# Performance work log

Hardware: AMD Instinct MI355X
Metric: run time of the kernel (lower is better)

Reference implementation:

```python
import jax, jax.numpy as jnp
import numpy as np

B, W, N, F_IN = 2, 8, 10000, 5
E = 80000
H = 128


def setup_inputs() -> dict:
    key = jax.random.key(0)
    ks = jax.random.split(key, 16)
    s = 0.05
    inp = {
        "x": jax.random.normal(ks[0], (B, W, N, F_IN), dtype=jnp.float32),
        "edge_index": jax.random.randint(ks[1], (2, E), 0, N, dtype=jnp.int64),
        # GCN layer 1 (in_features -> hidden) and layer 2 (hidden -> hidden)
        "gcn1_w": jax.random.normal(ks[2], (F_IN, H), dtype=jnp.float32) * s,
        "gcn1_b": jnp.zeros((H,), dtype=jnp.float32),
        "gcn2_w": jax.random.normal(ks[3], (H, H), dtype=jnp.float32) * s,
        "gcn2_b": jnp.zeros((H,), dtype=jnp.float32),
        # LSTM (torch gate order: i, f, g, o)
        "lstm_w_ih": jax.random.normal(ks[4], (4 * H, H), dtype=jnp.float32) * s,
        "lstm_w_hh": jax.random.normal(ks[5], (4 * H, H), dtype=jnp.float32) * s,
        "lstm_b_ih": jnp.zeros((4 * H,), dtype=jnp.float32),
        "lstm_b_hh": jnp.zeros((4 * H,), dtype=jnp.float32),
        # Decoder MLP: H -> H//2 -> 1
        "dec_w1": jax.random.normal(ks[6], (H, H // 2), dtype=jnp.float32) * s,
        "dec_b1": jnp.zeros((H // 2,), dtype=jnp.float32),
        "dec_w2": jax.random.normal(ks[7], (H // 2, 1), dtype=jnp.float32) * s,
        "dec_b2": jnp.zeros((1,), dtype=jnp.float32),
    }
    return inp


def _forward(x, edge_index, gcn1_w, gcn1_b, gcn2_w, gcn2_b,
             lstm_w_ih, lstm_w_hh, lstm_b_ih, lstm_b_hh,
             dec_w1, dec_b1, dec_w2, dec_b2):
    b, w, n, f_in = x.shape
    h_dim = gcn1_w.shape[1]
    # --- GCN normalization (PyG GCNConv default: add self-loops, sym-norm) ---
    loop = jnp.arange(n, dtype=edge_index.dtype)
    src = jnp.concatenate([edge_index[0], loop])
    dst = jnp.concatenate([edge_index[1], loop])
    deg = jnp.zeros((n,), x.dtype).at[dst].add(jnp.float32(1.0))
    dinv = jax.lax.rsqrt(deg)
    norm = dinv[src] * dinv[dst]  # (E+N,)

    def gcn(h, wm, bias):
        # h: (BW, N, Fin) -> (BW, N, H). Transform-then-aggregate (linear op).
        ht = h @ wm                                   # (BW, N, H)
        msg = ht[:, src, :] * norm[None, :, None]      # (BW, E+N, H)
        agg = jnp.zeros_like(ht).at[:, dst, :].add(msg)
        return agg + bias

    xf = x.reshape(b * w, n, f_in)
    h = jax.nn.relu(gcn(xf, gcn1_w, gcn1_b))   # dropout is identity at eval
    h = jax.nn.relu(gcn(h, gcn2_w, gcn2_b))

    # (BW, N, H) -> (B, N, W, H) -> (B*N, W, H): per-node temporal sequences
    h = h.reshape(b, w, n, h_dim).transpose(0, 2, 1, 3).reshape(b * n, w, h_dim)

    # --- single-layer LSTM, keep only last hidden state ---
    def step(carry, xt):
        hp, cp = carry
        gates = xt @ lstm_w_ih.T + hp @ lstm_w_hh.T + lstm_b_ih + lstm_b_hh
        i, f, g, o = jnp.split(gates, 4, axis=-1)
        c = jax.nn.sigmoid(f) * cp + jax.nn.sigmoid(i) * jnp.tanh(g)
        hn = jax.nn.sigmoid(o) * jnp.tanh(c)
        return (hn, c), None

    init = (jnp.zeros((b * n, h_dim), x.dtype), jnp.zeros((b * n, h_dim), x.dtype))
    (h_last, _), _ = jax.lax.scan(step, init, h.transpose(1, 0, 2))  # scan over W

    # --- MLP decoder ---
    d = jax.nn.relu(h_last @ dec_w1 + dec_b1)
    pred = (d @ dec_w2 + dec_b2)[..., 0]
    return pred.reshape(b, n)


def reference(x, edge_index, gcn1_w, gcn1_b, gcn2_w, gcn2_b,
              lstm_w_ih, lstm_w_hh, lstm_b_ih, lstm_b_hh,
              dec_w1, dec_b1, dec_w2, dec_b2):
    return _forward(x, edge_index, gcn1_w, gcn1_b, gcn2_w, gcn2_b,
                    lstm_w_ih, lstm_w_hh, lstm_b_ih, lstm_b_hh,
                    dec_w1, dec_b1, dec_w2, dec_b2)
```

## Files before the change

kernel.cpp:

```cpp
#include <hip/hip_runtime.h>
#include <hip/hip_fp16.h>
#include <cstdint>
#include <cstddef>

#define Bn   2
#define Wn   8
#define Nn   10000
#define Fin  5
#define En   80000
#define Hn   128
#define BWn  (Bn*Wn)
#define ROWS (BWn*Nn)
#define MR   (Bn*Nn)
#define LROWS 32

typedef _Float16 half8 __attribute__((ext_vector_type(8)));
typedef float f32x4 __attribute__((ext_vector_type(4)));

#define LOG2E 1.44269504088896f

__device__ __forceinline__ float fast_sigmoid(float x) {
    return __builtin_amdgcn_rcpf(1.f + __builtin_amdgcn_exp2f(-LOG2E * x));
}
__device__ __forceinline__ float fast_tanh(float x) {
    return fmaf(-2.f, __builtin_amdgcn_rcpf(1.f + __builtin_amdgcn_exp2f(2.f * LOG2E * x)), 1.f);
}

__global__ __launch_bounds__(256) void setup_kernel(
    const int* __restrict__ ei, const float* __restrict__ bih, const float* __restrict__ bhh,
    const float* __restrict__ wih, const float* __restrict__ whh,
    const float* __restrict__ g2w, const float* __restrict__ x,
    const float* __restrict__ dw1,
    int* __restrict__ counts, float* __restrict__ bsum,
    _Float16* __restrict__ wif, _Float16* __restrict__ whf,
    _Float16* __restrict__ g2wt, float* __restrict__ xt,
    _Float16* __restrict__ d1f) {
    __shared__ float buf[6400];
    const int b = blockIdx.x;
    const int tid = threadIdx.x;
    if (b < 313) {
        int e = b * 256 + tid;
        if (e < En) atomicAdd(&counts[ei[En + e]], 1);
    } else if (b < 315) {
        int i = (b - 313) * 256 + tid;
        if (i < 4 * Hn) bsum[i] = bih[i] + bhh[i];
    } else if (b < 891) {
        int i = (b - 315) * 256 + tid;
        if (i < 131072) {
            int idx = i & 65535;
            int j = idx & 7, lane = (idx >> 3) & 63, kt = (idx >> 9) & 3, ct = idx >> 11;
            int n = ct * 16 + (lane & 15);
            int k = kt * 32 + (lane >> 4) * 8 + j;
            if (i < 65536) wif[idx] = (_Float16)wih[n * 128 + k];
            else           whf[idx] = (_Float16)whh[n * 128 + k];
        } else {
            int j = i - 131072;
            int n = j >> 7, k = j & 127;
            g2wt[j] = (_Float16)g2w[k * Hn + n];
        }
    } else if (b < 1016) {
        const int n0 = (b - 891) * 80;
        for (int i = tid; i < 6400; i += 256) {
            int s = i / 400, r = i - s * 400;
            int node = r / 5, f = r - node * 5;
            buf[(node * 16 + s) * 5 + f] = x[((size_t)s * Nn + n0) * 5 + r];
        }
        __syncthreads();
        float* dst = xt + (size_t)n0 * 80;
        for (int i = tid; i < 6400; i += 256) dst[i] = buf[i];
    } else {
        int i = (b - 1016) * 256 + tid;
        int j = i & 7, lane = (i >> 3) & 63, kt = (i >> 9) & 3, ct = i >> 11;
        int n = ct * 16 + (lane & 15);
        int k = kt * 32 + (lane >> 4) * 8 + j;
        d1f[i] = (_Float16)dw1[k * 64 + n];
    }
}

enum { CHUNK = 10 };
static_assert(CHUNK * 1024 >= Nn, "scan chunk");

__global__ __launch_bounds__(1024) void scan_kernel(
    const int* __restrict__ counts, int* __restrict__ row_ptr,
    int* __restrict__ fill_ptr, float* __restrict__ dinv) {
    __shared__ int sums[1024];
    const int t = threadIdx.x;
    const int base = t * CHUNK;
    int cnt[CHUNK];
    int s = 0;
    #pragma unroll
    for (int i = 0; i < CHUNK; ++i) {
        int idx = base + i;
        int v = (idx < Nn) ? counts[idx] + 1 : 0;
        cnt[i] = v; s += v;
    }
    sums[t] = s;
    __syncthreads();
    for (int off = 1; off < 1024; off <<= 1) {
        int v = (t >= off) ? sums[t - off] : 0;
        __syncthreads();
        sums[t] += v;
        __syncthreads();
    }
    int excl = (t == 0) ? 0 : sums[t - 1];
    #pragma unroll
    for (int i = 0; i < CHUNK; ++i) {
        int idx = base + i;
        if (idx < Nn) {
            row_ptr[idx] = excl;
            fill_ptr[idx] = excl;
            dinv[idx] = rsqrtf((float)cnt[i]);
            excl += cnt[i];
        }
    }
    if (t == 1023) row_ptr[Nn] = excl;
}

__global__ void fill_kernel(const int* __restrict__ ei,
                            const float* __restrict__ dinv,
                            int* fill_ptr, int* __restrict__ col,
                            float* __restrict__ wgt) {
    int i = blockIdx.x * blockDim.x + threadIdx.x;
    if (i < Nn) {
        int p = atomicAdd(&fill_ptr[i], 1);
        col[p] = i;
        wgt[p] = dinv[i] * dinv[i];
    } else if (i < Nn + En) {
        int e = i - Nn;
        int s = ei[e];
        int d = ei[En + e];
        int p = atomicAdd(&fill_ptr[d], 1);
        col[p] = s;
        wgt[p] = dinv[s] * dinv[d];
    }
}

__global__ __launch_bounds__(256) void gcn2_fused_kernel(
    const float* __restrict__ xt, const int* __restrict__ row_ptr,
    const int* __restrict__ col, const float* __restrict__ wgt,
    const float* __restrict__ w1, const float* __restrict__ b1,
    const _Float16* __restrict__ g2wt, _Float16* __restrict__ C) {
    __shared__ float agg_lds[128 * 5];
    __shared__ __align__(16) _Float16 s_buf[128][136];
    __shared__ _Float16 Bs[128][40];
    const int tid = threadIdx.x;
    const int m0 = blockIdx.x * 128;
    const int n0 = m0 >> 4;
    {
        const int nl = tid >> 5;
        const int it = tid & 31;
        const int n = n0 + nl;
        const int start = row_ptr[n], end = row_ptr[n + 1];
        float a0 = 0.f, a1 = 0.f, a2 = 0.f;
        for (int e = start; e < end; ++e) {
            const float w = wgt[e];
            const float* src = xt + (size_t)col[e] * 80;
            a0 = fmaf(w, src[it], a0);
            a1 = fmaf(w, src[it + 32], a1);
            if (it < 16) a2 = fmaf(w, src[it + 64], a2);
        }
        agg_lds[nl * 80 + it] = a0;
        agg_lds[nl * 80 + it + 32] = a1;
        if (it < 16) agg_lds[nl * 80 + it + 64] = a2;
    }
    __syncthreads();
    {
        const int rg = tid >> 4;
        const int cg = tid & 15;
        float wreg[Fin][8], breg[8];
        #pragma unroll
        for (int k = 0; k < 8; ++k) breg[k] = b1[cg * 8 + k];
        #pragma unroll
        for (int f = 0; f < Fin; ++f)
            #pragma unroll
            for (int k = 0; k < 8; ++k) wreg[f][k] = w1[f * Hn + cg * 8 + k];
        #pragma unroll
        for (int rr = 0; rr < 8; ++rr) {
            const float* ar = &agg_lds[(rg * 8 + rr) * Fin];
            float a[Fin];
            #pragma unroll
            for (int f = 0; f < Fin; ++f) a[f] = ar[f];
            half8 v;
            #pragma unroll
            for (int k = 0; k < 8; ++k) {
                float s = breg[k];
                #pragma unroll
                for (int f = 0; f < Fin; ++f) s = fmaf(a[f], wreg[f][k], s);
                v[k] = (_Float16)fmaxf(s, 0.f);
            }
            *(half8*)&s_buf[rg * 8 + rr][cg * 8] = v;
        }
    }
    __syncthreads();
    const int wave = tid >> 6, lane = tid & 63;
    const int l = lane & 15, q = lane >> 4;
    const int wm = (wave & 1) * 64, wn = (wave >> 1) * 64;
    f32x4 acc[4][4];
    #pragma unroll
    for (int i = 0; i < 4; ++i)
        #pragma unroll
        for (int j = 0; j < 4; ++j) acc[i][j] = (f32x4){0.f, 0.f, 0.f, 0.f};
    for (int kt = 0; kt < 128; kt += 32) {
        #pragma unroll
        for (int j = 0; j < 2; ++j) {
            int idx = tid + j * 256;
            int r = idx >> 2, c = (idx & 3) * 8;
            *(half8*)&Bs[r][c] = *(const half8*)(g2wt + (size_t)r * 128 + kt + c);
        }
        __syncthreads();
        half8 af[4], bf[4];
        #pragma unroll
        for (int i = 0; i < 4; ++i) af[i] = *(const half8*)&s_buf[wm + i * 16 + l][kt + q * 8];
        #pragma unroll
        for (int j = 0; j < 4; ++j) bf[j] = *(const half8*)&Bs[wn + j * 16 + l][q * 8];
        #pragma unroll
        for (int i = 0; i < 4; ++i)
            #pragma unroll
            for (int j = 0; j < 4; ++j)
                acc[i][j] = __builtin_amdgcn_mfma_f32_16x16x32_f16(
                    af[i], bf[j], acc[i][j], 0, 0, 0);
        __syncthreads();
    }
    #pragma unroll
    for (int j = 0; j < 4; ++j) {
        int ccol = wn + j * 16 + l;
        #pragma unroll
        for (int i = 0; i < 4; ++i)
            #pragma unroll
            for (int r = 0; r < 4; ++r)
                s_buf[wm + i * 16 + q * 4 + r][ccol] = (_Float16)acc[i][j][r];
    }
    __syncthreads();
    const size_t base = (size_t)m0 * 128;
    #pragma unroll
    for (int it = 0; it < 8; ++it) {
        int idx = it * 256 + tid;
        int row = idx >> 4, ch = (idx & 15) * 8;
        *(half8*)(C + base + (size_t)row * 128 + ch) = *(const half8*)&s_buf[row][ch];
    }
}

__global__ __launch_bounds__(64) void gcn_agg2_kernel(
    const _Float16* __restrict__ ht, const int* __restrict__ row_ptr,
    const int* __restrict__ col, const float* __restrict__ wgt,
    const float* __restrict__ bias, _Float16* __restrict__ out) {
    const int n = blockIdx.x;
    const int t = threadIdx.x;
    const int s = blockIdx.y * 4 + (t >> 4);
    const int g = (t & 15) * 8;
    const int start = row_ptr[n], end = row_ptr[n + 1];
    const size_t lofs = (size_t)s * Hn + g;
    float acc[8];
    #pragma unroll
    for (int j = 0; j < 8; ++j) acc[j] = 0.f;
    int e = start;
    for (; e + 3 < end; e += 4) {
        const int c0 = col[e], c1 = col[e + 1], c2 = col[e + 2], c3 = col[e + 3];
        const float w0 = wgt[e], w1 = wgt[e + 1], w2 = wgt[e + 2], w3 = wgt[e + 3];
        half8 v0 = *(const half8*)(ht + (size_t)c0 * (BWn * Hn) + lofs);
        half8 v1 = *(const half8*)(ht + (size_t)c1 * (BWn * Hn) + lofs);
        half8 v2 = *(const half8*)(ht + (size_t)c2 * (BWn * Hn) + lofs);
        half8 v3 = *(const half8*)(ht + (size_t)c3 * (BWn * Hn) + lofs);
        #pragma unroll
        for (int j = 0; j < 8; ++j) {
            acc[j] = fmaf(w0, (float)v0[j], acc[j]);
            acc[j] = fmaf(w1, (float)v1[j], acc[j]);
            acc[j] = fmaf(w2, (float)v2[j], acc[j]);
            acc[j] = fmaf(w3, (float)v3[j], acc[j]);
        }
    }
    for (; e < end; ++e) {
        const float w = wgt[e];
        half8 v = *(const half8*)(ht + (size_t)col[e] * (BWn * Hn) + lofs);
        #pragma unroll
        for (int j = 0; j < 8; ++j) acc[j] = fmaf(w, (float)v[j], acc[j]);
    }
    half8 o;
    #pragma unroll
    for (int j = 0; j < 8; ++j) o[j] = (_Float16)fmaxf(acc[j] + bias[g + j], 0.f);
    *(half8*)(out + (size_t)n * (BWn * Hn) + lofs) = o;
}

__global__ __launch_bounds__(512, 1) void lstm_fused6_kernel(
    const _Float16* __restrict__ h2, const _Float16* __restrict__ wif,
    const _Float16* __restrict__ whf, const float* __restrict__ bsum,
    const _Float16* __restrict__ d1f, const float* __restrict__ db1,
    const float* __restrict__ dw2, const float* __restrict__ db2,
    float* __restrict__ out) {
    __shared__ __align__(16) _Float16 x_lds[2][LROWS][144];
    __shared__ __align__(16) _Float16 h_lds[2][LROWS][144];
    const int tid = threadIdx.x;
    const int nw = tid >> 6, lane = tid & 63;
    const int l = lane & 15, q = lane >> 4;
    const int r0 = blockIdx.x * LROWS;
    const int srow = tid >> 4, sch = (tid & 15) * 8;
    const int sgrow = r0 + srow;
    const int sb = (sgrow >= Nn) ? 1 : 0;
    const int sn = sgrow - sb * Nn;
    const _Float16* xbase = h2 + ((size_t)sn * BWn + sb * Wn) * 128 + sch;

    half8 wic[4][4], whc[4][4];
    #pragma unroll
    for (int g = 0; g < 4; ++g) {
        int ct = g * 8 + nw;
        #pragma unroll
        for (int kt = 0; kt < 4; ++kt) {
            wic[g][kt] = *(const half8*)(wif + (((size_t)ct * 4 + kt) * 64 + lane) * 8);
            whc[g][kt] = *(const half8*)(whf + (((size_t)ct * 4 + kt) * 64 + lane) * 8);
        }
    }
    float bias[4];
    #pragma unroll
    for (int g = 0; g < 4; ++g) bias[g] = bsum[g * 128 + nw * 16 + l];
    float c_reg[2][4];
    #pragma unroll
    for (int i = 0; i < 2; ++i)
        #pragma unroll
        for (int r = 0; r < 4; ++r) c_reg[i][r] = 0.f;

    *(half8*)&x_lds[0][srow][sch] = *(const half8*)(xbase);
    __syncthreads();

    for (int t = 0; t < Wn; ++t) {
        half8 xv = {0, 0, 0, 0, 0, 0, 0, 0};
        if (t + 1 < Wn) xv = *(const half8*)(xbase + (size_t)(t + 1) * 128);

        f32x4 acc[2][4];
        #pragma unroll
        for (int i = 0; i < 2; ++i)
            #pragma unroll
            for (int g = 0; g < 4; ++g)
                acc[i][g] = (f32x4){bias[g], bias[g], bias[g], bias[g]};

        #pragma unroll
        for (int kt = 0; kt < 4; ++kt) {
            half8 af[2];
            #pragma unroll
            for (int i = 0; i < 2; ++i)
                af[i] = *(const half8*)&x_lds[t & 1][i * 16 + l][kt * 32 + q * 8];
            #pragma unroll
            for (int i = 0; i < 2; ++i)
                #pragma unroll
                for (int g = 0; g < 4; ++g)
                    acc[i][g] = __builtin_amdgcn_mfma_f32_16x16x32_f16(
                        af[i], wic[g][kt], acc[i][g], 0, 0, 0);
        }
        if (t > 0) {
            #pragma unroll
            for (int kt = 0; kt < 4; ++kt) {
                half8 af[2];
                #pragma unroll
                for (int i = 0; i < 2; ++i)
                    af[i] = *(const half8*)&h_lds[t & 1][i * 16 + l][kt * 32 + q * 8];
                #pragma unroll
                for (int i = 0; i < 2; ++i)
                    #pragma unroll
                    for (int g = 0; g < 4; ++g)
                        acc[i][g] = __builtin_amdgcn_mfma_f32_16x16x32_f16(
                            af[i], whc[g][kt], acc[i][g], 0, 0, 0);
            }
        }

        #pragma unroll
        for (int i = 0; i < 2; ++i) {
            #pragma unroll
            for (int r = 0; r < 4; ++r) {
                float si = fast_sigmoid(acc[i][0][r]);
                float sf = fast_sigmoid(acc[i][1][r]);
                float tg = fast_tanh(acc[i][2][r]);
                float so = fast_sigmoid(acc[i][3][r]);
                float cn = sf * c_reg[i][r] + si * tg;
                c_reg[i][r] = cn;
                h_lds[(t + 1) & 1][i * 16 + q * 4 + r][nw * 16 + l] =
                    (_Float16)(so * fast_tanh(cn));
            }
        }
        if (t + 1 < Wn) *(half8*)&x_lds[(t + 1) & 1][srow][sch] = xv;
        __syncthreads();
    }

    const int mi = nw >> 2;
    const int ni = nw & 3;
    f32x4 dacc = (f32x4){0.f, 0.f, 0.f, 0.f};
    #pragma unroll
    for (int kt = 0; kt < 4; ++kt) {
        half8 af = *(const half8*)&h_lds[0][mi * 16 + l][kt * 32 + q * 8];
        half8 bf = *(const half8*)(d1f + (((size_t)ni * 4 + kt) * 64 + lane) * 8);
        dacc = __builtin_amdgcn_mfma_f32_16x16x32_f16(af, bf, dacc, 0, 0, 0);
    }
    const int unit = ni * 16 + l;
    const float bd1 = db1[unit];
    const float wd2 = dw2[unit];
    float pr[4];
    #pragma unroll
    for (int r = 0; r < 4; ++r)
        pr[r] = fmaxf(dacc[r] + bd1, 0.f) * wd2;
    #pragma unroll
    for (int m = 1; m < 16; m <<= 1)
        #pragma unroll
        for (int r = 0; r < 4; ++r)
            pr[r] += __shfl_xor(pr[r], m);
    float* part = (float*)&x_lds[0][0][0];
    if (l == 0) {
        #pragma unroll
        for (int r = 0; r < 4; ++r)
            part[(mi * 16 + q * 4 + r) * 4 + ni] = pr[r];
    }
    __syncthreads();
    if (tid < LROWS) {
        float s = part[tid * 4] + part[tid * 4 + 1] + part[tid * 4 + 2] + part[tid * 4 + 3];
        out[r0 + tid] = s + db2[0];
    }
}


extern "C" void kernel_launch(void* const* d_in, const int* in_sizes, int n_in,
                              void* d_out, int out_size, void* d_ws, size_t ws_size,
                              hipStream_t stream) {
    const float* x   = (const float*)d_in[0];
    const int*   ei  = (const int*)d_in[1];
    const float* g1w = (const float*)d_in[2];
    const float* g1b = (const float*)d_in[3];
    const float* g2w = (const float*)d_in[4];
    const float* g2b = (const float*)d_in[5];
    const float* wih = (const float*)d_in[6];
    const float* whh = (const float*)d_in[7];
    const float* bih = (const float*)d_in[8];
    const float* bhh = (const float*)d_in[9];
    const float* dw1 = (const float*)d_in[10];
    const float* db1 = (const float*)d_in[11];
    const float* dw2 = (const float*)d_in[12];
    const float* db2 = (const float*)d_in[13];
    float* out = (float*)d_out;

    char* p = (char*)d_ws;
    auto alloc = [&](size_t bytes) {
        char* r = p;
        p += (bytes + 255) & ~(size_t)255;
        return r;
    };
    int*      counts   = (int*)     alloc(Nn * 4);
    int*      row_ptr  = (int*)     alloc((Nn + 1) * 4);
    int*      fill_ptr = (int*)     alloc((Nn + 1) * 4);
    float*    dinv     = (float*)   alloc(Nn * 4);
    float*    bsum     = (float*)   alloc(4 * Hn * 4);
    int*      col      = (int*)     alloc((En + Nn) * 4);
    float*    wgt      = (float*)   alloc((En + Nn) * 4);
    _Float16* wif      = (_Float16*)alloc(512 * 128 * 2);
    _Float16* whf      = (_Float16*)alloc(512 * 128 * 2);
    _Float16* g2wt     = (_Float16*)alloc(128 * 128 * 2);
    _Float16* d1f      = (_Float16*)alloc(64 * 128 * 2);
    float*    xt       = (float*)   alloc((size_t)Nn * 80 * 4);
    _Float16* htf      = (_Float16*)alloc((size_t)ROWS * Hn * 2);
    _Float16* h2f      = (_Float16*)alloc((size_t)ROWS * Hn * 2);

    hipMemsetAsync(counts, 0, Nn * 4, stream);

    setup_kernel<<<1048, 256, 0, stream>>>(ei, bih, bhh, wih, whh, g2w, x, dw1,
                                           counts, bsum, wif, whf, g2wt, xt, d1f);
    scan_kernel<<<1, 1024, 0, stream>>>(counts, row_ptr, fill_ptr, dinv);
    fill_kernel<<<(Nn + En + 255) / 256, 256, 0, stream>>>(ei, dinv, fill_ptr, col, wgt);

    gcn2_fused_kernel<<<ROWS / 128, 256, 0, stream>>>(
        xt, row_ptr, col, wgt, g1w, g1b, g2wt, htf);

    gcn_agg2_kernel<<<dim3(Nn, 4), 64, 0, stream>>>(htf, row_ptr, col, wgt, g2b, h2f);

    lstm_fused6_kernel<<<MR / LROWS, 512, 0, stream>>>(
        h2f, wif, whf, bsum, d1f, db1, dw2, db2, out);
}
```

Measured before the change: 245.3 us.

## Fuse second GCN aggregation into LSTM kernel via per-timestep neighbor gather

Removes the standalone GCN layer-2 aggregation kernel and its intermediate h2 buffer. The LSTM kernel now computes each timestep's input row on the fly by gathering neighbor rows of the transformed features, applying edge weights, bias and ReLU. This saves a kernel launch and a full write and read of a 40 MB intermediate. In exchange the irregular gather latency now sits inside the serial LSTM loop, where only the next step's gather overlaps, in a kernel with one 512-thread block per CU.

```diff
diff --git a/kernel.cpp b/kernel.cpp
--- a/kernel.cpp
+++ b/kernel.cpp
@@ -240,50 +240,43 @@
     }
 }
 
-__global__ __launch_bounds__(64) void gcn_agg2_kernel(
-    const _Float16* __restrict__ ht, const int* __restrict__ row_ptr,
+__device__ __forceinline__ half8 gather_x(
+    const _Float16* __restrict__ htf, const int* __restrict__ col,
+    const float* __restrict__ wgt, int gstart, int gend,
+    int slice, int sch, const float* bg) {
+    float xa[8];
+    #pragma unroll
+    for (int j = 0; j < 8; ++j) xa[j] = 0.f;
+    int e = gstart;
+    for (; e + 1 < gend; e += 2) {
+        const int c0 = col[e], c1 = col[e + 1];
+        const float w0 = wgt[e], w1 = wgt[e + 1];
+        half8 v0 = *(const half8*)(htf + ((size_t)c0 * BWn + slice) * Hn + sch);
+        half8 v1 = *(const half8*)(htf + ((size_t)c1 * BWn + slice) * Hn + sch);
+        #pragma unroll
+        for (int j = 0; j < 8; ++j) {
+            xa[j] = fmaf(w0, (float)v0[j], xa[j]);
+            xa[j] = fmaf(w1, (float)v1[j], xa[j]);
+        }
+    }
+    if (e < gend) {
+        const float w = wgt[e];
+        half8 v = *(const half8*)(htf + ((size_t)col[e] * BWn + slice) * Hn + sch);
+        #pragma unroll
+        for (int j = 0; j < 8; ++j) xa[j] = fmaf(w, (float)v[j], xa[j]);
+    }
+    half8 xv;
+    #pragma unroll
+    for (int j = 0; j < 8; ++j) xv[j] = (_Float16)fmaxf(xa[j] + bg[j], 0.f);
+    return xv;
+}
+
+__global__ __launch_bounds__(512, 1) void lstm_fused7_kernel(
+    const _Float16* __restrict__ htf, const int* __restrict__ row_ptr,
     const int* __restrict__ col, const float* __restrict__ wgt,
-    const float* __restrict__ bias, _Float16* __restrict__ out) {
-    const int n = blockIdx.x;
-    const int t = threadIdx.x;
-    const int s = blockIdx.y * 4 + (t >> 4);
-    const int g = (t & 15) * 8;
-    const int start = row_ptr[n], end = row_ptr[n + 1];
-    const size_t lofs = (size_t)s * Hn + g;
-    float acc[8];
-    #pragma unroll
-    for (int j = 0; j < 8; ++j) acc[j] = 0.f;
-    int e = start;
-    for (; e + 3 < end; e += 4) {
-        const int c0 = col[e], c1 = col[e + 1], c2 = col[e + 2], c3 = col[e + 3];
-        const float w0 = wgt[e], w1 = wgt[e + 1], w2 = wgt[e + 2], w3 = wgt[e + 3];
-        half8 v0 = *(const half8*)(ht + (size_t)c0 * (BWn * Hn) + lofs);
-        half8 v1 = *(const half8*)(ht + (size_t)c1 * (BWn * Hn) + lofs);
-        half8 v2 = *(const half8*)(ht + (size_t)c2 * (BWn * Hn) + lofs);
-        half8 v3 = *(const half8*)(ht + (size_t)c3 * (BWn * Hn) + lofs);
-        #pragma unroll
-        for (int j = 0; j < 8; ++j) {
-            acc[j] = fmaf(w0, (float)v0[j], acc[j]);
-            acc[j] = fmaf(w1, (float)v1[j], acc[j]);
-            acc[j] = fmaf(w2, (float)v2[j], acc[j]);
-            acc[j] = fmaf(w3, (float)v3[j], acc[j]);
-        }
-    }
-    for (; e < end; ++e) {
-        const float w = wgt[e];
-        half8 v = *(const half8*)(ht + (size_t)col[e] * (BWn * Hn) + lofs);
-        #pragma unroll
-        for (int j = 0; j < 8; ++j) acc[j] = fmaf(w, (float)v[j], acc[j]);
-    }
-    half8 o;
-    #pragma unroll
-    for (int j = 0; j < 8; ++j) o[j] = (_Float16)fmaxf(acc[j] + bias[g + j], 0.f);
-    *(half8*)(out + (size_t)n * (BWn * Hn) + lofs) = o;
-}
-
-__global__ __launch_bounds__(512, 1) void lstm_fused6_kernel(
-    const _Float16* __restrict__ h2, const _Float16* __restrict__ wif,
-    const _Float16* __restrict__ whf, const float* __restrict__ bsum,
+    const float* __restrict__ g2b,
+    const _Float16* __restrict__ wif, const _Float16* __restrict__ whf,
+    const float* __restrict__ bsum,
     const _Float16* __restrict__ d1f, const float* __restrict__ db1,
     const float* __restrict__ dw2, const float* __restrict__ db2,
     float* __restrict__ out) {
@@ -297,7 +290,10 @@
     const int sgrow = r0 + srow;
     const int sb = (sgrow >= Nn) ? 1 : 0;
     const int sn = sgrow - sb * Nn;
-    const _Float16* xbase = h2 + ((size_t)sn * BWn + sb * Wn) * 128 + sch;
+    const int gstart = row_ptr[sn], gend = row_ptr[sn + 1];
+    float bg[8];
+    #pragma unroll
+    for (int j = 0; j < 8; ++j) bg[j] = g2b[sch + j];
 
     half8 wic[4][4], whc[4][4];
     #pragma unroll
@@ -318,13 +314,11 @@
         #pragma unroll
         for (int r = 0; r < 4; ++r) c_reg[i][r] = 0.f;
 
-    *(half8*)&x_lds[0][srow][sch] = *(const half8*)(xbase);
+    *(half8*)&x_lds[0][srow][sch] =
+        gather_x(htf, col, wgt, gstart, gend, sb * Wn, sch, bg);
     __syncthreads();
 
     for (int t = 0; t < Wn; ++t) {
-        half8 xv = {0, 0, 0, 0, 0, 0, 0, 0};
-        if (t + 1 < Wn) xv = *(const half8*)(xbase + (size_t)(t + 1) * 128);
-
         f32x4 acc[2][4];
         #pragma unroll
         for (int i = 0; i < 2; ++i)
@@ -375,7 +369,9 @@
                     (_Float16)(so * fast_tanh(cn));
             }
         }
-        if (t + 1 < Wn) *(half8*)&x_lds[(t + 1) & 1][srow][sch] = xv;
+        if (t + 1 < Wn)
+            *(half8*)&x_lds[(t + 1) & 1][srow][sch] =
+                gather_x(htf, col, wgt, gstart, gend, sb * Wn + t + 1, sch, bg);
         __syncthreads();
     }
 
@@ -452,7 +448,6 @@
     _Float16* d1f      = (_Float16*)alloc(64 * 128 * 2);
     float*    xt       = (float*)   alloc((size_t)Nn * 80 * 4);
     _Float16* htf      = (_Float16*)alloc((size_t)ROWS * Hn * 2);
-    _Float16* h2f      = (_Float16*)alloc((size_t)ROWS * Hn * 2);
 
     hipMemsetAsync(counts, 0, Nn * 4, stream);
 
@@ -464,8 +459,6 @@
     gcn2_fused_kernel<<<ROWS / 128, 256, 0, stream>>>(
         xt, row_ptr, col, wgt, g1w, g1b, g2wt, htf);
 
-    gcn_agg2_kernel<<<dim3(Nn, 4), 64, 0, stream>>>(htf, row_ptr, col, wgt, g2b, h2f);
-
-    lstm_fused6_kernel<<<MR / LROWS, 512, 0, stream>>>(
-        h2f, wif, whf, bsum, d1f, db1, dw2, db2, out);
-}
+    lstm_fused7_kernel<<<MR / LROWS, 512, 0, stream>>>(
+        htf, row_ptr, col, wgt, g2b, wif, whf, bsum, d1f, db1, dw2, db2, out);
+}
```

Measured after the change: 322.2 us. 31.4% more time.
